# Kernel tuning notes

Measured on AMD Instinct MI355X. Metric: run time of the kernel, lower is better.

## Reference

```python
import jax, jax.numpy as jnp
import numpy as np
from jax import lax

B, NBB, C, H, W = 32, 16, 1024, 22, 22
P = 3            # pooled output size (3x3)
SCALE = 1.0 / 16.0
EPS = 1e-5


def setup_inputs() -> dict:
    key = jax.random.key(0)
    ks = jax.random.split(key, 12)
    feat = jax.random.normal(ks[0], (B, C, H, W), jnp.float32)
    # bbox in xywh image coords, in-range for a 352x352 search region
    xy = jax.random.uniform(ks[1], (B, NBB, 2), jnp.float32, 0.0, 250.0)
    wh = jax.random.uniform(ks[2], (B, NBB, 2), jnp.float32, 16.0, 100.0)
    bbox = jnp.concatenate([xy, wh], axis=-1)
    conv_w = jax.random.normal(ks[3], (C, C, 3, 3), jnp.float32) * 0.01
    conv_b = jnp.zeros((C,), jnp.float32)
    bn_gamma = jnp.ones((C,), jnp.float32)
    bn_beta = jnp.zeros((C,), jnp.float32)
    bn_mean = jax.random.normal(ks[4], (C,), jnp.float32) * 0.1
    bn_var = jax.random.uniform(ks[5], (C,), jnp.float32, 0.5, 1.5)
    w1 = jax.random.normal(ks[6], (C // 2, C), jnp.float32) * 0.02
    b1 = jnp.zeros((C // 2,), jnp.float32)
    w2 = jax.random.normal(ks[7], (C // 2, C // 2), jnp.float32) * 0.02
    b2 = jnp.zeros((C // 2,), jnp.float32)
    w3 = jax.random.normal(ks[8], (512, C // 2), jnp.float32) * 0.02
    b3 = jnp.zeros((512,), jnp.float32)
    return dict(feat=feat, bbox=bbox, conv_w=conv_w, conv_b=conv_b,
                bn_gamma=bn_gamma, bn_beta=bn_beta, bn_mean=bn_mean, bn_var=bn_var,
                w1=w1, b1=b1, w2=w2, b2=b2, w3=w3, b3=b3)


def _hat_int(t):
    # Antiderivative of the bilinear hat h(u)=max(0,1-|u|), clipped to support.
    t = jnp.clip(t, -1.0, 1.0)
    return t + 0.5 - 0.5 * t * jnp.abs(t)


def _bin_weights(lo, bw, n):
    # lo, bw: [B, NBB].  Returns exact integral weights [B, NBB, P, n]:
    # W[b,r,p,i] = integral over bin p of hat(x - i) dx  (PrRoI closed form).
    p = jnp.arange(P, dtype=lo.dtype)
    xs = lo[..., None] + p * bw[..., None]          # [B,NBB,P] bin starts
    xe = xs + bw[..., None]                          # bin ends
    i = jnp.arange(n, dtype=lo.dtype)
    return _hat_int(xe[..., None] - i) - _hat_int(xs[..., None] - i)


def reference(feat, bbox, conv_w, conv_b, bn_gamma, bn_beta, bn_mean, bn_var,
              w1, b1, w2, b2, w3, b3):
    # --- PrRoI pooling (exact separable bilinear integral) ---
    x1 = bbox[..., 0] * SCALE
    y1 = bbox[..., 1] * SCALE
    x2 = (bbox[..., 0] + bbox[..., 2]) * SCALE
    y2 = (bbox[..., 1] + bbox[..., 3]) * SCALE
    bw = (x2 - x1) / P
    bh = (y2 - y1) / P
    Wx = _bin_weights(x1, bw, W)                     # [B,NBB,P,W]
    Wy = _bin_weights(y1, bh, H)                     # [B,NBB,P,H]
    pooled = jnp.einsum('bchw,bnqh,bnpw->bncqp', feat, Wy, Wx)  # [B,NBB,C,P,P]
    area = jnp.maximum(bw * bh, 0.0)[..., None, None, None]
    pooled = jnp.where(area > 0, pooled / jnp.maximum(area, 1e-12), 0.0)
    x = pooled.reshape(B * NBB, C, P, P)

    # --- conv_bn_relu: 3x3 conv, valid padding -> 1x1, BN (eval), ReLU ---
    x = lax.conv_general_dilated(x, conv_w, (1, 1), 'VALID',
                                 dimension_numbers=('NCHW', 'OIHW', 'NCHW'))
    x = x + conv_b[:, None, None]
    x = (x - bn_mean[:, None, None]) * (bn_gamma * lax.rsqrt(bn_var + EPS))[:, None, None]
    x = x + bn_beta[:, None, None]
    x = jax.nn.relu(x)

    # --- MLP head ---
    x = x.reshape(B * NBB, C)
    x = jax.nn.relu(x @ w1.T + b1)
    x = jax.nn.relu(x @ w2.T + b2)
    x = x @ w3.T + b3
    return x.reshape(B, NBB, 512)
```

## Files before the change

### kernel.cpp

```cpp
#include <hip/hip_runtime.h>
#include <hip/hip_bf16.h>

#define B_    32
#define NBB_  16
#define C_    1024
#define NROI  512
#define KCONV 9216
#define SCALE_ (1.0f/16.0f)
#define EPS_  1e-5f

using f32x4  = __attribute__((ext_vector_type(4))) float;
using bf16x8 = __attribute__((ext_vector_type(8))) short;

__device__ __forceinline__ unsigned f2bf(float f) {
  union { float f; unsigned u; } x; x.f = f;
  unsigned r = x.u + 0x7fffu + ((x.u >> 16) & 1u);
  return r >> 16;
}

__device__ __forceinline__ float hat_int(float t) {
  t = fminf(fmaxf(t, -1.f), 1.f);
  return t + 0.5f - 0.5f * t * fabsf(t);
}

__device__ __forceinline__ void glds16(const void* g, void* l) {
  __builtin_amdgcn_global_load_lds((const __attribute__((address_space(1))) void*)g,
                                   (__attribute__((address_space(3))) void*)l, 16, 0, 0);
}

__global__ __launch_bounds__(32) void prep_rois(const float* __restrict__ bbox,
                                                float* __restrict__ wy,
                                                float* __restrict__ wx) {
  int r = blockIdx.x;
  float4 bb = ((const float4*)bbox)[r];
  float x1 = bb.x * SCALE_, y1 = bb.y * SCALE_;
  float x2 = (bb.x + bb.z) * SCALE_, y2 = (bb.y + bb.w) * SCALE_;
  float bw = (x2 - x1) / 3.f, bh = (y2 - y1) / 3.f;
  float area = fmaxf(bw * bh, 0.f);
  float inv = area > 0.f ? 1.f / fmaxf(area, 1e-12f) : 0.f;
  int i = threadIdx.x;
  if (i < 22) {
    float fi = (float)i;
#pragma unroll
    for (int q = 0; q < 3; ++q) {
      float sy = y1 + q * bh;
      wy[r*66 + q*22 + i] = hat_int(sy + bh - fi) - hat_int(sy - fi);
      float sx = x1 + q * bw;
      wx[r*66 + q*22 + i] = (hat_int(sx + bw - fi) - hat_int(sx - fi)) * inv;
    }
  }
}

__global__ __launch_bounds__(256) void cvt_bf16(const float* __restrict__ src,
                                                unsigned short* __restrict__ dst, int n8) {
  int i = blockIdx.x * 256 + threadIdx.x;
  if (i >= n8) return;
  float4 a = ((const float4*)src)[2*i];
  float4 b = ((const float4*)src)[2*i + 1];
  uint4 pk;
  pk.x = f2bf(a.x) | (f2bf(a.y) << 16);
  pk.y = f2bf(a.z) | (f2bf(a.w) << 16);
  pk.z = f2bf(b.x) | (f2bf(b.y) << 16);
  pk.w = f2bf(b.z) | (f2bf(b.w) << 16);
  ((uint4*)dst)[i] = pk;
}

__global__ __launch_bounds__(256) void convw_t(const float* __restrict__ cw,
                                               unsigned short* __restrict__ out) {
  __shared__ float T[9][260];
  int o = blockIdx.x, cc = blockIdx.y;
  int tid = threadIdx.x;
  const float* src = cw + (size_t)o * 9216 + (size_t)cc * 2304;
  for (int i = tid; i < 576; i += 256) {
    float4 v = ((const float4*)src)[i];
    int e = i * 4;
#pragma unroll
    for (int j = 0; j < 4; ++j) {
      int ee = e + j;
      int c = ee / 9, qp = ee - c * 9;
      T[qp][c] = ((const float*)&v)[j];
    }
  }
  __syncthreads();
  unsigned short* dst = out + (size_t)o * 9216 + cc * 256 + tid;
#pragma unroll
  for (int qp = 0; qp < 9; ++qp) dst[qp * 1024] = (unsigned short)f2bf(T[qp][tid]);
}

__global__ __launch_bounds__(192) void w2d_build(const float* __restrict__ wy,
                                                 const float* __restrict__ wx,
                                                 unsigned short* __restrict__ W2d) {
  __shared__ float wyS[1056], wxS[1056];
  int b = blockIdx.x, tid = threadIdx.x;
  for (int i = tid; i < 1056; i += 192) { wyS[i] = wy[(size_t)b*1056 + i]; wxS[i] = wx[(size_t)b*1056 + i]; }
  __syncthreads();
  if (tid < 144) {
    int n = tid / 9, qp = tid - n*9, q = qp / 3, p = qp - q*3;
    const float* wyp = wyS + n*66 + q*22;
    const float* wxp = wxS + n*66 + p*22;
    unsigned short* out = W2d + ((size_t)b*144 + tid) * 512;
    for (int h = 0; h < 22; ++h) {
      float yv = wyp[h];
      int kb = h * 22;
#pragma unroll
      for (int w = 0; w < 22; w += 2) {
        unsigned pk = f2bf(yv * wxp[w]) | (f2bf(yv * wxp[w+1]) << 16);
        *(unsigned*)&out[kb + w] = pk;
      }
    }
    for (int k = 484; k < 512; k += 2) *(unsigned*)&out[k] = 0u;
  }
}

__global__ __launch_bounds__(384) void pool_gemm(const float* __restrict__ feat,
                                                 const unsigned short* __restrict__ W2d,
                                                 unsigned short* __restrict__ X) {
  __shared__ __align__(16) unsigned short As[144 * 72];
  __shared__ __align__(16) unsigned short Bs[64 * 72];
  int tid = threadIdx.x;
  int nch = blockIdx.x, b = blockIdx.y;
  int lane = tid & 63, wid = tid >> 6;
  int wm = wid >> 1, wn = wid & 1;
  int l15 = lane & 15, kg = lane >> 4;
  const unsigned short* w2b = W2d + (size_t)b * 144 * 512;
  const float* fb = feat + ((size_t)b * C_ + (size_t)nch * 64) * 484;
  f32x4 acc[3][2] = {};

  for (int s = 0; s < 8; ++s) {
    __syncthreads();
#pragma unroll
    for (int t = 0; t < 3; ++t) {
      int i = tid + t * 384;
      int row = i >> 3, slot = i & 7;
      uint4 v = *(const uint4*)(w2b + (size_t)row * 512 + s * 64 + slot * 8);
      *(uint4*)&As[row * 72 + slot * 8] = v;
    }
    for (int i = tid; i < 1024; i += 384) {
      int c = i >> 4, f4 = i & 15;
      float4 v;
      if (s < 7 || f4 <= 8) v = *(const float4*)(fb + (size_t)c * 484 + s * 64 + f4 * 4);
      else v = make_float4(0.f, 0.f, 0.f, 0.f);
      uint2 pk;
      pk.x = f2bf(v.x) | (f2bf(v.y) << 16);
      pk.y = f2bf(v.z) | (f2bf(v.w) << 16);
      *(uint2*)&Bs[c * 72 + f4 * 4] = pk;
    }
    __syncthreads();

    bf16x8 af[3][2], bf[2][2];
#pragma unroll
    for (int fm = 0; fm < 3; ++fm)
#pragma unroll
      for (int kk = 0; kk < 2; ++kk)
        af[fm][kk] = *(const bf16x8*)&As[(wm*48 + fm*16 + l15) * 72 + kk*32 + kg*8];
#pragma unroll
    for (int fn = 0; fn < 2; ++fn)
#pragma unroll
      for (int kk = 0; kk < 2; ++kk)
        bf[fn][kk] = *(const bf16x8*)&Bs[(wn*32 + fn*16 + l15) * 72 + kk*32 + kg*8];
#pragma unroll
    for (int fm = 0; fm < 3; ++fm)
#pragma unroll
      for (int fn = 0; fn < 2; ++fn) {
        acc[fm][fn] = __builtin_amdgcn_mfma_f32_16x16x32_bf16(af[fm][0], bf[fn][0], acc[fm][fn], 0, 0, 0);
        acc[fm][fn] = __builtin_amdgcn_mfma_f32_16x16x32_bf16(af[fm][1], bf[fn][1], acc[fm][fn], 0, 0, 0);
      }
  }

#pragma unroll
  for (int fm = 0; fm < 3; ++fm)
#pragma unroll
    for (int r = 0; r < 4; ++r) {
      int m = wm*48 + fm*16 + kg*4 + r;
      int n = m / 9, qp = m - n*9;
      size_t base = ((size_t)(b*16 + n)) * KCONV + (size_t)qp * 1024 + (size_t)nch * 64;
#pragma unroll
      for (int fn = 0; fn < 2; ++fn)
        X[base + wn*32 + fn*16 + l15] = (unsigned short)f2bf(acc[fm][fn][r]);
    }
}

__global__ __launch_bounds__(256) void gemm128(const unsigned short* __restrict__ A,
                                               const unsigned short* __restrict__ Bm,
                                               float* __restrict__ Cp,
                                               int M, int N, int K, int kChunk) {
  __shared__ __align__(16) unsigned short As[2][4096];
  __shared__ __align__(16) unsigned short Bs[2][4096];
  int tid = threadIdx.x;
  int lane = tid & 63, wid = tid >> 6;
  int wm = wid >> 1, wn = wid & 1;
  int l15 = lane & 15, kg = lane >> 4;
  int nt = blockIdx.x, mt = blockIdx.y, z = blockIdx.z;
  int kbeg = z * kChunk;
  int steps = kChunk / 32;

  int row0 = tid >> 2, row1 = 64 + row0;
  int slot = tid & 3;
  int s0 = slot ^ ((row0 >> 1) & 3);
  int s1 = slot ^ ((row1 >> 1) & 3);
  const unsigned short* ga0 = A  + (size_t)(mt*128 + row0) * K + kbeg + s0*8;
  const unsigned short* ga1 = A  + (size_t)(mt*128 + row1) * K + kbeg + s1*8;
  const unsigned short* gb0 = Bm + (size_t)(nt*128 + row0) * K + kbeg + s0*8;
  const unsigned short* gb1 = Bm + (size_t)(nt*128 + row1) * K + kbeg + s1*8;
  int wbyte = wid * 1024;

  f32x4 acc[4][4] = {};
  int cur = 0;

#define ISSUE(buf, s) do { int ko = (s) * 32; \
    glds16(ga0 + ko, (char*)&As[(buf)][0] + wbyte); \
    glds16(ga1 + ko, (char*)&As[(buf)][0] + 4096 + wbyte); \
    glds16(gb0 + ko, (char*)&Bs[(buf)][0] + wbyte); \
    glds16(gb1 + ko, (char*)&Bs[(buf)][0] + 4096 + wbyte); } while (0)

  ISSUE(0, 0);
  for (int s = 0; s < steps; ++s) {
    __syncthreads();
    if (s + 1 < steps) ISSUE(cur ^ 1, s + 1);
    bf16x8 af[4], bfr[4];
#pragma unroll
    for (int fm = 0; fm < 4; ++fm) {
      int fr = wm*64 + fm*16 + l15;
      af[fm] = *(const bf16x8*)&As[cur][fr*32 + ((kg ^ ((fr >> 1) & 3)) << 3)];
    }
#pragma unroll
    for (int fn = 0; fn < 4; ++fn) {
      int fr = wn*64 + fn*16 + l15;
      bfr[fn] = *(const bf16x8*)&Bs[cur][fr*32 + ((kg ^ ((fr >> 1) & 3)) << 3)];
    }
#pragma unroll
    for (int fm = 0; fm < 4; ++fm)
#pragma unroll
      for (int fn = 0; fn < 4; ++fn)
        acc[fm][fn] = __builtin_amdgcn_mfma_f32_16x16x32_bf16(af[fm], bfr[fn], acc[fm][fn], 0, 0, 0);
    cur ^= 1;
  }
#undef ISSUE

  float* cp = Cp + ((size_t)z * M + (size_t)mt * 128) * N + (size_t)nt * 128;
#pragma unroll
  for (int fm = 0; fm < 4; ++fm)
#pragma unroll
    for (int fn = 0; fn < 4; ++fn)
#pragma unroll
      for (int r = 0; r < 4; ++r) {
        int row = wm*64 + fm*16 + kg*4 + r;
        int col = wn*64 + fn*16 + l15;
        cp[(size_t)row * N + col] = acc[fm][fn][r];
      }
}

__global__ __launch_bounds__(256) void gemm_nt(const unsigned short* __restrict__ A,
                                               const unsigned short* __restrict__ Bm,
                                               float* __restrict__ Cp,
                                               int M, int N, int K, int kChunk) {
  __shared__ __align__(16) unsigned short As[64][40];
  __shared__ __align__(16) unsigned short Bs[64][40];
  int tid = threadIdx.x;
  int lane = tid & 63, wid = tid >> 6;
  int wm = wid >> 1, wn = wid & 1;
  int l15 = lane & 15, kg = lane >> 4;
  int nt = blockIdx.x, mt = blockIdx.y, z = blockIdx.z;
  int kbeg = z * kChunk;
  int kend = kbeg + kChunk; if (kend > K) kend = K;
  int srow = tid >> 2, sseg = tid & 3;
  const unsigned short* aG = A  + (size_t)(mt*64 + srow) * K + sseg * 8;
  const unsigned short* bG = Bm + (size_t)(nt*64 + srow) * K + sseg * 8;
  f32x4 acc[2][2] = {};

  for (int k0 = kbeg; k0 < kend; k0 += 32) {
    uint4 av = *(const uint4*)(aG + k0);
    uint4 bv = *(const uint4*)(bG + k0);
    __syncthreads();
    *(uint4*)&As[srow][sseg*8] = av;
    *(uint4*)&Bs[srow][sseg*8] = bv;
    __syncthreads();
    bf16x8 a0 = *(const bf16x8*)&As[wm*32 +      l15][kg*8];
    bf16x8 a1 = *(const bf16x8*)&As[wm*32 + 16 + l15][kg*8];
    bf16x8 b0 = *(const bf16x8*)&Bs[wn*32 +      l15][kg*8];
    bf16x8 b1 = *(const bf16x8*)&Bs[wn*32 + 16 + l15][kg*8];
    acc[0][0] = __builtin_amdgcn_mfma_f32_16x16x32_bf16(a0, b0, acc[0][0], 0, 0, 0);
    acc[0][1] = __builtin_amdgcn_mfma_f32_16x16x32_bf16(a0, b1, acc[0][1], 0, 0, 0);
    acc[1][0] = __builtin_amdgcn_mfma_f32_16x16x32_bf16(a1, b0, acc[1][0], 0, 0, 0);
    acc[1][1] = __builtin_amdgcn_mfma_f32_16x16x32_bf16(a1, b1, acc[1][1], 0, 0, 0);
  }

  float* cp = Cp + ((size_t)z * M + (size_t)mt * 64) * N + (size_t)nt * 64;
#pragma unroll
  for (int fm = 0; fm < 2; ++fm)
#pragma unroll
    for (int fn = 0; fn < 2; ++fn)
#pragma unroll
      for (int r = 0; r < 4; ++r) {
        int row = wm*32 + fm*16 + kg*4 + r;
        int col = wn*32 + fn*16 + l15;
        cp[(size_t)row * N + col] = acc[fm][fn][r];
      }
}

template<int MODE>
__global__ __launch_bounds__(256) void epi(const float* __restrict__ Cp, int SK, int MN4, int N,
                                           const float* __restrict__ bias,
                                           const float* __restrict__ g,
                                           const float* __restrict__ be,
                                           const float* __restrict__ mu,
                                           const float* __restrict__ var,
                                           unsigned short* __restrict__ outb,
                                           float* __restrict__ outf) {
  int i = blockIdx.x * 256 + threadIdx.x;
  if (i >= MN4) return;
  float4 s = ((const float4*)Cp)[i];
  for (int z = 1; z < SK; ++z) {
    float4 t = ((const float4*)Cp)[(size_t)z * MN4 + i];
    s.x += t.x; s.y += t.y; s.z += t.z; s.w += t.w;
  }
  int n0 = (i * 4) % N;
  float v[4] = {s.x, s.y, s.z, s.w};
  if (MODE == 0) {
    unsigned o[4];
#pragma unroll
    for (int j = 0; j < 4; ++j) {
      int n = n0 + j;
      float sc = g[n] * rsqrtf(var[n] + EPS_);
      float t = (v[j] + bias[n] - mu[n]) * sc + be[n];
      o[j] = f2bf(fmaxf(t, 0.f));
    }
    uint2 pk; pk.x = o[0] | (o[1] << 16); pk.y = o[2] | (o[3] << 16);
    *(uint2*)&outb[(size_t)i * 4] = pk;
  } else if (MODE == 1) {
    unsigned o[4];
#pragma unroll
    for (int j = 0; j < 4; ++j) o[j] = f2bf(fmaxf(v[j] + bias[n0 + j], 0.f));
    uint2 pk; pk.x = o[0] | (o[1] << 16); pk.y = o[2] | (o[3] << 16);
    *(uint2*)&outb[(size_t)i * 4] = pk;
  } else {
    float4 o;
    o.x = v[0] + bias[n0];     o.y = v[1] + bias[n0 + 1];
    o.z = v[2] + bias[n0 + 2]; o.w = v[3] + bias[n0 + 3];
    ((float4*)outf)[i] = o;
  }
}

extern "C" void kernel_launch(void* const* d_in, const int* in_sizes, int n_in,
                              void* d_out, int out_size, void* d_ws, size_t ws_size,
                              hipStream_t stream) {
  const float* feat   = (const float*)d_in[0];
  const float* bbox   = (const float*)d_in[1];
  const float* conv_w = (const float*)d_in[2];
  const float* conv_b = (const float*)d_in[3];
  const float* gamma  = (const float*)d_in[4];
  const float* beta   = (const float*)d_in[5];
  const float* mean   = (const float*)d_in[6];
  const float* var    = (const float*)d_in[7];
  const float* w1     = (const float*)d_in[8];
  const float* b1     = (const float*)d_in[9];
  const float* w2     = (const float*)d_in[10];
  const float* b2     = (const float*)d_in[11];
  const float* w3     = (const float*)d_in[12];
  const float* b3     = (const float*)d_in[13];

  char* ws = (char*)d_ws;
  float*          wy  = (float*)(ws);
  float*          wx  = (float*)(ws + 135168);
  unsigned short* W2d = (unsigned short*)(ws + 270336);
  unsigned short* H0  = (unsigned short*)(ws);
  unsigned short* H1  = (unsigned short*)(ws + 1048576);
  unsigned short* H2  = (unsigned short*)(ws + 1572864);
  unsigned short* Xb  = (unsigned short*)(ws + 4988928);
  unsigned short* Wfb = (unsigned short*)(ws + 14426112);
  unsigned short* w1b = (unsigned short*)(ws + 33300480);
  unsigned short* w2b = (unsigned short*)(ws + 34349056);
  unsigned short* w3b = (unsigned short*)(ws + 34873344);
  float*          part= (float*)(ws + 35397632);

  prep_rois<<<NROI, 32, 0, stream>>>(bbox, wy, wx);
  w2d_build<<<32, 192, 0, stream>>>(wy, wx, W2d);
  convw_t<<<dim3(1024, 4), 256, 0, stream>>>(conv_w, Wfb);
  cvt_bf16<<<(65536 + 255) / 256, 256, 0, stream>>>(w1, w1b, 65536);
  cvt_bf16<<<(32768 + 255) / 256, 256, 0, stream>>>(w2, w2b, 32768);
  cvt_bf16<<<(32768 + 255) / 256, 256, 0, stream>>>(w3, w3b, 32768);

  pool_gemm<<<dim3(16, 32), 384, 0, stream>>>(feat, W2d, Xb);

  gemm128<<<dim3(8, 4, 6), 256, 0, stream>>>(Xb, Wfb, part, 512, 1024, 9216, 1536);
  epi<0><<<(131072 + 255) / 256, 256, 0, stream>>>(part, 6, 131072, 1024,
      conv_b, gamma, beta, mean, var, H0, nullptr);

  gemm_nt<<<dim3(8, 8, 4), 256, 0, stream>>>(H0, w1b, part, 512, 512, 1024, 256);
  epi<1><<<(65536 + 255) / 256, 256, 0, stream>>>(part, 4, 65536, 512,
      b1, nullptr, nullptr, nullptr, nullptr, H1, nullptr);

  gemm_nt<<<dim3(8, 8, 4), 256, 0, stream>>>(H1, w2b, part, 512, 512, 512, 128);
  epi<1><<<(65536 + 255) / 256, 256, 0, stream>>>(part, 4, 65536, 512,
      b2, nullptr, nullptr, nullptr, nullptr, H2, nullptr);

  gemm_nt<<<dim3(8, 8, 4), 256, 0, stream>>>(H2, w3b, part, 512, 512, 512, 128);
  epi<2><<<(65536 + 255) / 256, 256, 0, stream>>>(part, 4, 65536, 512,
      b3, nullptr, nullptr, nullptr, nullptr, nullptr, (float*)d_out);
}
```

Measured before the change: 134.5 us.

## Fuse ROI prep kernels, register-prefetch pool GEMM, restructure conv-weight transpose, deepen split-K

Merges prep_rois and w2d_build into one kernel so the hat weights stay in shared memory. The conv-weight transpose is reworked to one block per output channel, storing bf16 in LDS with vectorized writes. pool_gemm now prefetches the next feature tile into registers and reads the A operand straight from global memory instead of staging it in LDS. The conv GEMM split-K goes from 6 to 8 slices, and bf16 packing switches to the hardware pair conversion intrinsic. Together these cut launches, LDS traffic and load latency, at the cost of uncached global A reads and a larger partial-sum reduction.

```diff
diff --git a/kernel.cpp b/kernel.cpp
--- a/kernel.cpp
+++ b/kernel.cpp
@@ -18,6 +18,11 @@
   return r >> 16;
 }
 
+__device__ __forceinline__ unsigned pk_bf16(float lo, float hi) {
+  __hip_bfloat162 h = __float22bfloat162_rn(make_float2(lo, hi));
+  return *reinterpret_cast<unsigned*>(&h);
+}
+
 __device__ __forceinline__ float hat_int(float t) {
   t = fminf(fmaxf(t, -1.f), 1.f);
   return t + 0.5f - 0.5f * t * fabsf(t);
@@ -28,71 +33,27 @@
                                    (__attribute__((address_space(3))) void*)l, 16, 0, 0);
 }
 
-__global__ __launch_bounds__(32) void prep_rois(const float* __restrict__ bbox,
-                                                float* __restrict__ wy,
-                                                float* __restrict__ wx) {
-  int r = blockIdx.x;
-  float4 bb = ((const float4*)bbox)[r];
-  float x1 = bb.x * SCALE_, y1 = bb.y * SCALE_;
-  float x2 = (bb.x + bb.z) * SCALE_, y2 = (bb.y + bb.w) * SCALE_;
-  float bw = (x2 - x1) / 3.f, bh = (y2 - y1) / 3.f;
-  float area = fmaxf(bw * bh, 0.f);
-  float inv = area > 0.f ? 1.f / fmaxf(area, 1e-12f) : 0.f;
-  int i = threadIdx.x;
-  if (i < 22) {
+__global__ __launch_bounds__(192) void prep_w2d(const float* __restrict__ bbox,
+                                                unsigned short* __restrict__ W2d) {
+  __shared__ float wyS[16*66], wxS[16*66];
+  int b = blockIdx.x, tid = threadIdx.x;
+  for (int t = tid; t < 352; t += 192) {
+    int n = t / 22, i = t - n * 22;
+    float4 bb = ((const float4*)bbox)[b*16 + n];
+    float x1 = bb.x * SCALE_, y1 = bb.y * SCALE_;
+    float x2 = (bb.x + bb.z) * SCALE_, y2 = (bb.y + bb.w) * SCALE_;
+    float bw = (x2 - x1) / 3.f, bh = (y2 - y1) / 3.f;
+    float area = fmaxf(bw * bh, 0.f);
+    float inv = area > 0.f ? 1.f / fmaxf(area, 1e-12f) : 0.f;
     float fi = (float)i;
 #pragma unroll
     for (int q = 0; q < 3; ++q) {
       float sy = y1 + q * bh;
-      wy[r*66 + q*22 + i] = hat_int(sy + bh - fi) - hat_int(sy - fi);
+      wyS[n*66 + q*22 + i] = hat_int(sy + bh - fi) - hat_int(sy - fi);
       float sx = x1 + q * bw;
-      wx[r*66 + q*22 + i] = (hat_int(sx + bw - fi) - hat_int(sx - fi)) * inv;
-    }
-  }
-}
-
-__global__ __launch_bounds__(256) void cvt_bf16(const float* __restrict__ src,
-                                                unsigned short* __restrict__ dst, int n8) {
-  int i = blockIdx.x * 256 + threadIdx.x;
-  if (i >= n8) return;
-  float4 a = ((const float4*)src)[2*i];
-  float4 b = ((const float4*)src)[2*i + 1];
-  uint4 pk;
-  pk.x = f2bf(a.x) | (f2bf(a.y) << 16);
-  pk.y = f2bf(a.z) | (f2bf(a.w) << 16);
-  pk.z = f2bf(b.x) | (f2bf(b.y) << 16);
-  pk.w = f2bf(b.z) | (f2bf(b.w) << 16);
-  ((uint4*)dst)[i] = pk;
-}
-
-__global__ __launch_bounds__(256) void convw_t(const float* __restrict__ cw,
-                                               unsigned short* __restrict__ out) {
-  __shared__ float T[9][260];
-  int o = blockIdx.x, cc = blockIdx.y;
-  int tid = threadIdx.x;
-  const float* src = cw + (size_t)o * 9216 + (size_t)cc * 2304;
-  for (int i = tid; i < 576; i += 256) {
-    float4 v = ((const float4*)src)[i];
-    int e = i * 4;
-#pragma unroll
-    for (int j = 0; j < 4; ++j) {
-      int ee = e + j;
-      int c = ee / 9, qp = ee - c * 9;
-      T[qp][c] = ((const float*)&v)[j];
-    }
-  }
-  __syncthreads();
-  unsigned short* dst = out + (size_t)o * 9216 + cc * 256 + tid;
-#pragma unroll
-  for (int qp = 0; qp < 9; ++qp) dst[qp * 1024] = (unsigned short)f2bf(T[qp][tid]);
-}
-
-__global__ __launch_bounds__(192) void w2d_build(const float* __restrict__ wy,
-                                                 const float* __restrict__ wx,
-                                                 unsigned short* __restrict__ W2d) {
-  __shared__ float wyS[1056], wxS[1056];
-  int b = blockIdx.x, tid = threadIdx.x;
-  for (int i = tid; i < 1056; i += 192) { wyS[i] = wy[(size_t)b*1056 + i]; wxS[i] = wx[(size_t)b*1056 + i]; }
+      wxS[n*66 + q*22 + i] = (hat_int(sx + bw - fi) - hat_int(sx - fi)) * inv;
+    }
+  }
   __syncthreads();
   if (tid < 144) {
     int n = tid / 9, qp = tid - n*9, q = qp / 3, p = qp - q*3;
@@ -103,19 +64,56 @@
       float yv = wyp[h];
       int kb = h * 22;
 #pragma unroll
-      for (int w = 0; w < 22; w += 2) {
-        unsigned pk = f2bf(yv * wxp[w]) | (f2bf(yv * wxp[w+1]) << 16);
-        *(unsigned*)&out[kb + w] = pk;
-      }
-    }
+      for (int w = 0; w < 22; w += 2)
+        *(unsigned*)&out[kb + w] = pk_bf16(yv * wxp[w], yv * wxp[w+1]);
+    }
+#pragma unroll
     for (int k = 484; k < 512; k += 2) *(unsigned*)&out[k] = 0u;
+  }
+}
+
+__global__ __launch_bounds__(256) void cvt_bf16(const float* __restrict__ src,
+                                                unsigned short* __restrict__ dst, int n8) {
+  int i = blockIdx.x * 256 + threadIdx.x;
+  if (i >= n8) return;
+  float4 a = ((const float4*)src)[2*i];
+  float4 b = ((const float4*)src)[2*i + 1];
+  uint4 pk;
+  pk.x = pk_bf16(a.x, a.y); pk.y = pk_bf16(a.z, a.w);
+  pk.z = pk_bf16(b.x, b.y); pk.w = pk_bf16(b.z, b.w);
+  ((uint4*)dst)[i] = pk;
+}
+
+__global__ __launch_bounds__(256) void convw_t(const float* __restrict__ cw,
+                                               unsigned short* __restrict__ out) {
+  __shared__ unsigned short T[9][1028];
+  int o = blockIdx.x, tid = threadIdx.x;
+  const float4* src = (const float4*)(cw + (size_t)o * 9216);
+#pragma unroll
+  for (int it = 0; it < 9; ++it) {
+    int i = tid + it * 256;
+    float4 v = src[i];
+    int e = i * 4;
+    {
+      int c = e / 9, qp = e - c * 9;
+      T[qp][c] = (unsigned short)f2bf(v.x);
+    }
+    { int ee = e+1; int c = ee / 9, qp = ee - c * 9; T[qp][c] = (unsigned short)f2bf(v.y); }
+    { int ee = e+2; int c = ee / 9, qp = ee - c * 9; T[qp][c] = (unsigned short)f2bf(v.z); }
+    { int ee = e+3; int c = ee / 9, qp = ee - c * 9; T[qp][c] = (unsigned short)f2bf(v.w); }
+  }
+  __syncthreads();
+  unsigned short* dst = out + (size_t)o * 9216;
+#pragma unroll
+  for (int qp = 0; qp < 9; ++qp) {
+    uint2 w = *(const uint2*)&T[qp][tid * 4];
+    ((uint2*)(dst + qp * 1024))[tid] = w;
   }
 }
 
 __global__ __launch_bounds__(384) void pool_gemm(const float* __restrict__ feat,
                                                  const unsigned short* __restrict__ W2d,
                                                  unsigned short* __restrict__ X) {
-  __shared__ __align__(16) unsigned short As[144 * 72];
   __shared__ __align__(16) unsigned short Bs[64 * 72];
   int tid = threadIdx.x;
   int nch = blockIdx.x, b = blockIdx.y;
@@ -126,25 +124,32 @@
   const float* fb = feat + ((size_t)b * C_ + (size_t)nch * 64) * 484;
   f32x4 acc[3][2] = {};
 
+  int c0 = tid >> 4,        f40 = tid & 15;
+  int i1 = tid + 384;  int c1 = i1 >> 4, f41 = i1 & 15;
+  int i2 = tid + 768;  bool has2 = i2 < 1024; int c2 = i2 >> 4, f42 = i2 & 15;
+  float4 bR0, bR1, bR2;
+
+#define LOADB(s) do { \
+    bR0 = (((s) < 7 || f40 <= 8) ? *(const float4*)(fb + (size_t)c0*484 + (s)*64 + f40*4) : make_float4(0,0,0,0)); \
+    bR1 = (((s) < 7 || f41 <= 8) ? *(const float4*)(fb + (size_t)c1*484 + (s)*64 + f41*4) : make_float4(0,0,0,0)); \
+    if (has2) bR2 = (((s) < 7 || f42 <= 8) ? *(const float4*)(fb + (size_t)c2*484 + (s)*64 + f42*4) : make_float4(0,0,0,0)); \
+  } while (0)
+
+  LOADB(0);
+#pragma unroll
   for (int s = 0; s < 8; ++s) {
     __syncthreads();
-#pragma unroll
-    for (int t = 0; t < 3; ++t) {
-      int i = tid + t * 384;
-      int row = i >> 3, slot = i & 7;
-      uint4 v = *(const uint4*)(w2b + (size_t)row * 512 + s * 64 + slot * 8);
-      *(uint4*)&As[row * 72 + slot * 8] = v;
-    }
-    for (int i = tid; i < 1024; i += 384) {
-      int c = i >> 4, f4 = i & 15;
-      float4 v;
-      if (s < 7 || f4 <= 8) v = *(const float4*)(fb + (size_t)c * 484 + s * 64 + f4 * 4);
-      else v = make_float4(0.f, 0.f, 0.f, 0.f);
-      uint2 pk;
-      pk.x = f2bf(v.x) | (f2bf(v.y) << 16);
-      pk.y = f2bf(v.z) | (f2bf(v.w) << 16);
-      *(uint2*)&Bs[c * 72 + f4 * 4] = pk;
-    }
+    {
+      uint2 p0; p0.x = pk_bf16(bR0.x, bR0.y); p0.y = pk_bf16(bR0.z, bR0.w);
+      *(uint2*)&Bs[c0*72 + f40*4] = p0;
+      uint2 p1; p1.x = pk_bf16(bR1.x, bR1.y); p1.y = pk_bf16(bR1.z, bR1.w);
+      *(uint2*)&Bs[c1*72 + f41*4] = p1;
+      if (has2) {
+        uint2 p2; p2.x = pk_bf16(bR2.x, bR2.y); p2.y = pk_bf16(bR2.z, bR2.w);
+        *(uint2*)&Bs[c2*72 + f42*4] = p2;
+      }
+    }
+    if (s < 7) LOADB(s + 1);
     __syncthreads();
 
     bf16x8 af[3][2], bf[2][2];
@@ -152,7 +157,7 @@
     for (int fm = 0; fm < 3; ++fm)
 #pragma unroll
       for (int kk = 0; kk < 2; ++kk)
-        af[fm][kk] = *(const bf16x8*)&As[(wm*48 + fm*16 + l15) * 72 + kk*32 + kg*8];
+        af[fm][kk] = *(const bf16x8*)(w2b + (size_t)(wm*48 + fm*16 + l15) * 512 + s*64 + kk*32 + kg*8);
 #pragma unroll
     for (int fn = 0; fn < 2; ++fn)
 #pragma unroll
@@ -166,6 +171,7 @@
         acc[fm][fn] = __builtin_amdgcn_mfma_f32_16x16x32_bf16(af[fm][1], bf[fn][1], acc[fm][fn], 0, 0, 0);
       }
   }
+#undef LOADB
 
 #pragma unroll
   for (int fm = 0; fm < 3; ++fm)
@@ -317,21 +323,19 @@
   int n0 = (i * 4) % N;
   float v[4] = {s.x, s.y, s.z, s.w};
   if (MODE == 0) {
-    unsigned o[4];
+    float o[4];
 #pragma unroll
     for (int j = 0; j < 4; ++j) {
       int n = n0 + j;
       float sc = g[n] * rsqrtf(var[n] + EPS_);
-      float t = (v[j] + bias[n] - mu[n]) * sc + be[n];
-      o[j] = f2bf(fmaxf(t, 0.f));
-    }
-    uint2 pk; pk.x = o[0] | (o[1] << 16); pk.y = o[2] | (o[3] << 16);
+      o[j] = fmaxf((v[j] + bias[n] - mu[n]) * sc + be[n], 0.f);
+    }
+    uint2 pk; pk.x = pk_bf16(o[0], o[1]); pk.y = pk_bf16(o[2], o[3]);
     *(uint2*)&outb[(size_t)i * 4] = pk;
   } else if (MODE == 1) {
-    unsigned o[4];
-#pragma unroll
-    for (int j = 0; j < 4; ++j) o[j] = f2bf(fmaxf(v[j] + bias[n0 + j], 0.f));
-    uint2 pk; pk.x = o[0] | (o[1] << 16); pk.y = o[2] | (o[3] << 16);
+    uint2 pk;
+    pk.x = pk_bf16(fmaxf(v[0] + bias[n0], 0.f),     fmaxf(v[1] + bias[n0+1], 0.f));
+    pk.y = pk_bf16(fmaxf(v[2] + bias[n0+2], 0.f),   fmaxf(v[3] + bias[n0+3], 0.f));
     *(uint2*)&outb[(size_t)i * 4] = pk;
   } else {
     float4 o;
@@ -360,30 +364,27 @@
   const float* b3     = (const float*)d_in[13];
 
   char* ws = (char*)d_ws;
-  float*          wy  = (float*)(ws);
-  float*          wx  = (float*)(ws + 135168);
-  unsigned short* W2d = (unsigned short*)(ws + 270336);
-  unsigned short* H0  = (unsigned short*)(ws);
-  unsigned short* H1  = (unsigned short*)(ws + 1048576);
-  unsigned short* H2  = (unsigned short*)(ws + 1572864);
-  unsigned short* Xb  = (unsigned short*)(ws + 4988928);
-  unsigned short* Wfb = (unsigned short*)(ws + 14426112);
-  unsigned short* w1b = (unsigned short*)(ws + 33300480);
-  unsigned short* w2b = (unsigned short*)(ws + 34349056);
-  unsigned short* w3b = (unsigned short*)(ws + 34873344);
-  float*          part= (float*)(ws + 35397632);
-
-  prep_rois<<<NROI, 32, 0, stream>>>(bbox, wy, wx);
-  w2d_build<<<32, 192, 0, stream>>>(wy, wx, W2d);
-  convw_t<<<dim3(1024, 4), 256, 0, stream>>>(conv_w, Wfb);
+  unsigned short* W2d = (unsigned short*)(ws);
+  unsigned short* Xb  = (unsigned short*)(ws + 4718592);
+  unsigned short* Wfb = (unsigned short*)(ws + 14155776);
+  unsigned short* w1b = (unsigned short*)(ws + 33030144);
+  unsigned short* w2b = (unsigned short*)(ws + 34078720);
+  unsigned short* w3b = (unsigned short*)(ws + 34603008);
+  float*          part= (float*)(ws + 35127296);
+  unsigned short* H0  = (unsigned short*)(ws + 51904512);
+  unsigned short* H1  = (unsigned short*)(ws + 52953088);
+  unsigned short* H2  = (unsigned short*)(ws + 53477376);
+
+  prep_w2d<<<32, 192, 0, stream>>>(bbox, W2d);
+  convw_t<<<1024, 256, 0, stream>>>(conv_w, Wfb);
   cvt_bf16<<<(65536 + 255) / 256, 256, 0, stream>>>(w1, w1b, 65536);
   cvt_bf16<<<(32768 + 255) / 256, 256, 0, stream>>>(w2, w2b, 32768);
   cvt_bf16<<<(32768 + 255) / 256, 256, 0, stream>>>(w3, w3b, 32768);
 
   pool_gemm<<<dim3(16, 32), 384, 0, stream>>>(feat, W2d, Xb);
 
-  gemm128<<<dim3(8, 4, 6), 256, 0, stream>>>(Xb, Wfb, part, 512, 1024, 9216, 1536);
-  epi<0><<<(131072 + 255) / 256, 256, 0, stream>>>(part, 6, 131072, 1024,
+  gemm128<<<dim3(8, 4, 8), 256, 0, stream>>>(Xb, Wfb, part, 512, 1024, 9216, 1152);
+  epi<0><<<(131072 + 255) / 256, 256, 0, stream>>>(part, 8, 131072, 1024,
       conv_b, gamma, beta, mean, var, H0, nullptr);
 
   gemm_nt<<<dim3(8, 8, 4), 256, 0, stream>>>(H0, w1b, part, 512, 512, 1024, 256);
```

Result: faster. 126.8 us (-5.7%).

## Prefetch feature tiles in pool_gemm, fuse weight casts, widen conv split-K

Applied to the files above, without the earlier changes.

The pool_gemm kernel now keeps the next k-step's feature float4s in registers, loading them while the current tile is in LDS, and reads the W2d A fragments directly from global memory instead of staging them through shared memory. The three bf16 weight-conversion kernels are merged into one launch. Manual bf16 rounding is replaced with the packed hardware conversion intrinsic. The conv GEMM split-K goes from 6 to 8 chunks, and the H buffers move so they no longer alias the partial-sum region. The trade-offs are higher register pressure, uncached global A-fragment loads, and more partial sums for the epilogue to reduce.

```diff
diff --git a/kernel.cpp b/kernel.cpp
--- a/kernel.cpp
+++ b/kernel.cpp
@@ -16,6 +16,11 @@
   union { float f; unsigned u; } x; x.f = f;
   unsigned r = x.u + 0x7fffu + ((x.u >> 16) & 1u);
   return r >> 16;
+}
+
+__device__ __forceinline__ unsigned pk_bf16(float lo, float hi) {
+  __hip_bfloat162 h = __float22bfloat162_rn(make_float2(lo, hi));
+  return *reinterpret_cast<unsigned*>(&h);
 }
 
 __device__ __forceinline__ float hat_int(float t) {
@@ -49,42 +54,6 @@
       wx[r*66 + q*22 + i] = (hat_int(sx + bw - fi) - hat_int(sx - fi)) * inv;
     }
   }
-}
-
-__global__ __launch_bounds__(256) void cvt_bf16(const float* __restrict__ src,
-                                                unsigned short* __restrict__ dst, int n8) {
-  int i = blockIdx.x * 256 + threadIdx.x;
-  if (i >= n8) return;
-  float4 a = ((const float4*)src)[2*i];
-  float4 b = ((const float4*)src)[2*i + 1];
-  uint4 pk;
-  pk.x = f2bf(a.x) | (f2bf(a.y) << 16);
-  pk.y = f2bf(a.z) | (f2bf(a.w) << 16);
-  pk.z = f2bf(b.x) | (f2bf(b.y) << 16);
-  pk.w = f2bf(b.z) | (f2bf(b.w) << 16);
-  ((uint4*)dst)[i] = pk;
-}
-
-__global__ __launch_bounds__(256) void convw_t(const float* __restrict__ cw,
-                                               unsigned short* __restrict__ out) {
-  __shared__ float T[9][260];
-  int o = blockIdx.x, cc = blockIdx.y;
-  int tid = threadIdx.x;
-  const float* src = cw + (size_t)o * 9216 + (size_t)cc * 2304;
-  for (int i = tid; i < 576; i += 256) {
-    float4 v = ((const float4*)src)[i];
-    int e = i * 4;
-#pragma unroll
-    for (int j = 0; j < 4; ++j) {
-      int ee = e + j;
-      int c = ee / 9, qp = ee - c * 9;
-      T[qp][c] = ((const float*)&v)[j];
-    }
-  }
-  __syncthreads();
-  unsigned short* dst = out + (size_t)o * 9216 + cc * 256 + tid;
-#pragma unroll
-  for (int qp = 0; qp < 9; ++qp) dst[qp * 1024] = (unsigned short)f2bf(T[qp][tid]);
 }
 
 __global__ __launch_bounds__(192) void w2d_build(const float* __restrict__ wy,
@@ -103,19 +72,55 @@
       float yv = wyp[h];
       int kb = h * 22;
 #pragma unroll
-      for (int w = 0; w < 22; w += 2) {
-        unsigned pk = f2bf(yv * wxp[w]) | (f2bf(yv * wxp[w+1]) << 16);
-        *(unsigned*)&out[kb + w] = pk;
-      }
+      for (int w = 0; w < 22; w += 2)
+        *(unsigned*)&out[kb + w] = pk_bf16(yv * wxp[w], yv * wxp[w+1]);
     }
     for (int k = 484; k < 512; k += 2) *(unsigned*)&out[k] = 0u;
   }
+}
+
+__global__ __launch_bounds__(256) void cvt3_bf16(const float* __restrict__ w1, const float* __restrict__ w2,
+                                                 const float* __restrict__ w3,
+                                                 unsigned short* __restrict__ o1, unsigned short* __restrict__ o2,
+                                                 unsigned short* __restrict__ o3) {
+  int i = blockIdx.x * 256 + threadIdx.x;
+  const float* src; unsigned short* dst; int g;
+  if (i < 65536)      { src = w1; dst = o1; g = i; }
+  else if (i < 98304) { src = w2; dst = o2; g = i - 65536; }
+  else                { src = w3; dst = o3; g = i - 98304; }
+  float4 a = ((const float4*)src)[2*g];
+  float4 b = ((const float4*)src)[2*g + 1];
+  uint4 pk;
+  pk.x = pk_bf16(a.x, a.y); pk.y = pk_bf16(a.z, a.w);
+  pk.z = pk_bf16(b.x, b.y); pk.w = pk_bf16(b.z, b.w);
+  ((uint4*)dst)[g] = pk;
+}
+
+__global__ __launch_bounds__(256) void convw_t(const float* __restrict__ cw,
+                                               unsigned short* __restrict__ out) {
+  __shared__ float T[9][260];
+  int o = blockIdx.x, cc = blockIdx.y;
+  int tid = threadIdx.x;
+  const float* src = cw + (size_t)o * 9216 + (size_t)cc * 2304;
+  for (int i = tid; i < 576; i += 256) {
+    float4 v = ((const float4*)src)[i];
+    int e = i * 4;
+#pragma unroll
+    for (int j = 0; j < 4; ++j) {
+      int ee = e + j;
+      int c = ee / 9, qp = ee - c * 9;
+      T[qp][c] = ((const float*)&v)[j];
+    }
+  }
+  __syncthreads();
+  unsigned short* dst = out + (size_t)o * 9216 + cc * 256 + tid;
+#pragma unroll
+  for (int qp = 0; qp < 9; ++qp) dst[qp * 1024] = (unsigned short)f2bf(T[qp][tid]);
 }
 
 __global__ __launch_bounds__(384) void pool_gemm(const float* __restrict__ feat,
                                                  const unsigned short* __restrict__ W2d,
                                                  unsigned short* __restrict__ X) {
-  __shared__ __align__(16) unsigned short As[144 * 72];
   __shared__ __align__(16) unsigned short Bs[64 * 72];
   int tid = threadIdx.x;
   int nch = blockIdx.x, b = blockIdx.y;
@@ -126,25 +131,32 @@
   const float* fb = feat + ((size_t)b * C_ + (size_t)nch * 64) * 484;
   f32x4 acc[3][2] = {};
 
+  int c0 = tid >> 4,        f40 = tid & 15;
+  int i1 = tid + 384;  int c1 = i1 >> 4, f41 = i1 & 15;
+  int i2 = tid + 768;  bool has2 = i2 < 1024; int c2 = i2 >> 4, f42 = i2 & 15;
+  float4 bR0, bR1, bR2;
+
+#define LOADB(s) do { \
+    bR0 = (((s) < 7 || f40 <= 8) ? *(const float4*)(fb + (size_t)c0*484 + (s)*64 + f40*4) : make_float4(0,0,0,0)); \
+    bR1 = (((s) < 7 || f41 <= 8) ? *(const float4*)(fb + (size_t)c1*484 + (s)*64 + f41*4) : make_float4(0,0,0,0)); \
+    if (has2) bR2 = (((s) < 7 || f42 <= 8) ? *(const float4*)(fb + (size_t)c2*484 + (s)*64 + f42*4) : make_float4(0,0,0,0)); \
+  } while (0)
+
+  LOADB(0);
+#pragma unroll
   for (int s = 0; s < 8; ++s) {
     __syncthreads();
-#pragma unroll
-    for (int t = 0; t < 3; ++t) {
-      int i = tid + t * 384;
-      int row = i >> 3, slot = i & 7;
-      uint4 v = *(const uint4*)(w2b + (size_t)row * 512 + s * 64 + slot * 8);
-      *(uint4*)&As[row * 72 + slot * 8] = v;
-    }
-    for (int i = tid; i < 1024; i += 384) {
-      int c = i >> 4, f4 = i & 15;
-      float4 v;
-      if (s < 7 || f4 <= 8) v = *(const float4*)(fb + (size_t)c * 484 + s * 64 + f4 * 4);
-      else v = make_float4(0.f, 0.f, 0.f, 0.f);
-      uint2 pk;
-      pk.x = f2bf(v.x) | (f2bf(v.y) << 16);
-      pk.y = f2bf(v.z) | (f2bf(v.w) << 16);
-      *(uint2*)&Bs[c * 72 + f4 * 4] = pk;
-    }
+    {
+      uint2 p0; p0.x = pk_bf16(bR0.x, bR0.y); p0.y = pk_bf16(bR0.z, bR0.w);
+      *(uint2*)&Bs[c0*72 + f40*4] = p0;
+      uint2 p1; p1.x = pk_bf16(bR1.x, bR1.y); p1.y = pk_bf16(bR1.z, bR1.w);
+      *(uint2*)&Bs[c1*72 + f41*4] = p1;
+      if (has2) {
+        uint2 p2; p2.x = pk_bf16(bR2.x, bR2.y); p2.y = pk_bf16(bR2.z, bR2.w);
+        *(uint2*)&Bs[c2*72 + f42*4] = p2;
+      }
+    }
+    if (s < 7) LOADB(s + 1);
     __syncthreads();
 
     bf16x8 af[3][2], bf[2][2];
@@ -152,7 +164,7 @@
     for (int fm = 0; fm < 3; ++fm)
 #pragma unroll
       for (int kk = 0; kk < 2; ++kk)
-        af[fm][kk] = *(const bf16x8*)&As[(wm*48 + fm*16 + l15) * 72 + kk*32 + kg*8];
+        af[fm][kk] = *(const bf16x8*)(w2b + (size_t)(wm*48 + fm*16 + l15) * 512 + s*64 + kk*32 + kg*8);
 #pragma unroll
     for (int fn = 0; fn < 2; ++fn)
 #pragma unroll
@@ -166,6 +178,7 @@
         acc[fm][fn] = __builtin_amdgcn_mfma_f32_16x16x32_bf16(af[fm][1], bf[fn][1], acc[fm][fn], 0, 0, 0);
       }
   }
+#undef LOADB
 
 #pragma unroll
   for (int fm = 0; fm < 3; ++fm)
@@ -317,21 +330,19 @@
   int n0 = (i * 4) % N;
   float v[4] = {s.x, s.y, s.z, s.w};
   if (MODE == 0) {
-    unsigned o[4];
+    float o[4];
 #pragma unroll
     for (int j = 0; j < 4; ++j) {
       int n = n0 + j;
       float sc = g[n] * rsqrtf(var[n] + EPS_);
-      float t = (v[j] + bias[n] - mu[n]) * sc + be[n];
-      o[j] = f2bf(fmaxf(t, 0.f));
-    }
-    uint2 pk; pk.x = o[0] | (o[1] << 16); pk.y = o[2] | (o[3] << 16);
+      o[j] = fmaxf((v[j] + bias[n] - mu[n]) * sc + be[n], 0.f);
+    }
+    uint2 pk; pk.x = pk_bf16(o[0], o[1]); pk.y = pk_bf16(o[2], o[3]);
     *(uint2*)&outb[(size_t)i * 4] = pk;
   } else if (MODE == 1) {
-    unsigned o[4];
-#pragma unroll
-    for (int j = 0; j < 4; ++j) o[j] = f2bf(fmaxf(v[j] + bias[n0 + j], 0.f));
-    uint2 pk; pk.x = o[0] | (o[1] << 16); pk.y = o[2] | (o[3] << 16);
+    uint2 pk;
+    pk.x = pk_bf16(fmaxf(v[0] + bias[n0], 0.f),   fmaxf(v[1] + bias[n0+1], 0.f));
+    pk.y = pk_bf16(fmaxf(v[2] + bias[n0+2], 0.f), fmaxf(v[3] + bias[n0+3], 0.f));
     *(uint2*)&outb[(size_t)i * 4] = pk;
   } else {
     float4 o;
@@ -363,27 +374,25 @@
   float*          wy  = (float*)(ws);
   float*          wx  = (float*)(ws + 135168);
   unsigned short* W2d = (unsigned short*)(ws + 270336);
-  unsigned short* H0  = (unsigned short*)(ws);
-  unsigned short* H1  = (unsigned short*)(ws + 1048576);
-  unsigned short* H2  = (unsigned short*)(ws + 1572864);
   unsigned short* Xb  = (unsigned short*)(ws + 4988928);
   unsigned short* Wfb = (unsigned short*)(ws + 14426112);
   unsigned short* w1b = (unsigned short*)(ws + 33300480);
   unsigned short* w2b = (unsigned short*)(ws + 34349056);
   unsigned short* w3b = (unsigned short*)(ws + 34873344);
   float*          part= (float*)(ws + 35397632);
+  unsigned short* H0  = (unsigned short*)(ws + 52174848);
+  unsigned short* H1  = (unsigned short*)(ws + 53223424);
+  unsigned short* H2  = (unsigned short*)(ws + 53747712);
 
   prep_rois<<<NROI, 32, 0, stream>>>(bbox, wy, wx);
   w2d_build<<<32, 192, 0, stream>>>(wy, wx, W2d);
   convw_t<<<dim3(1024, 4), 256, 0, stream>>>(conv_w, Wfb);
-  cvt_bf16<<<(65536 + 255) / 256, 256, 0, stream>>>(w1, w1b, 65536);
-  cvt_bf16<<<(32768 + 255) / 256, 256, 0, stream>>>(w2, w2b, 32768);
-  cvt_bf16<<<(32768 + 255) / 256, 256, 0, stream>>>(w3, w3b, 32768);
+  cvt3_bf16<<<512, 256, 0, stream>>>(w1, w2, w3, w1b, w2b, w3b);
 
   pool_gemm<<<dim3(16, 32), 384, 0, stream>>>(feat, W2d, Xb);
 
-  gemm128<<<dim3(8, 4, 6), 256, 0, stream>>>(Xb, Wfb, part, 512, 1024, 9216, 1536);
-  epi<0><<<(131072 + 255) / 256, 256, 0, stream>>>(part, 6, 131072, 1024,
+  gemm128<<<dim3(8, 4, 8), 256, 0, stream>>>(Xb, Wfb, part, 512, 1024, 9216, 1152);
+  epi<0><<<(131072 + 255) / 256, 256, 0, stream>>>(part, 8, 131072, 1024,
       conv_b, gamma, beta, mean, var, H0, nullptr);
 
   gemm_nt<<<dim3(8, 8, 4), 256, 0, stream>>>(H0, w1b, part, 512, 512, 1024, 256);
```

After: 129.4 us. 1.04x faster.
